# Kernel optimization log

Hardware: AMD Instinct MI355X
Metric: run time of the kernel (lower is better)

The kernel has to match this reference:

```python
import jax, jax.numpy as jnp
import numpy as np

B, V, M, L, D, OUT = 16, 16, 32, 24, 128, 193
VOCAB = {'cond': 5000, 'proc': 2000, 'drug': 600, 'lab_item': 700, 'lab_value': 200, 'inj_item': 400, 'inj_value': 200}


def setup_inputs() -> dict:
    key = jax.random.key(0)
    ks = iter(jax.random.split(key, 48))
    def emb_table(v):
        t = 0.02 * jax.random.normal(next(ks), (v, D), jnp.float32)
        return t.at[0].set(0.0)  # padding_idx = 0
    inp = {}
    inp['tok_cond'] = jax.random.randint(next(ks), (B, V, L), 0, VOCAB['cond'])
    inp['tok_proc'] = jax.random.randint(next(ks), (B, V, L), 0, VOCAB['proc'])
    inp['tok_drug'] = jax.random.randint(next(ks), (B, V, L), 0, VOCAB['drug'])
    inp['tok_lab_item'] = jax.random.randint(next(ks), (B, V, M, L), 0, VOCAB['lab_item'])
    inp['tok_lab_value'] = jax.random.randint(next(ks), (B, V, M, L), 0, VOCAB['lab_value'])
    inp['tok_inj_item'] = jax.random.randint(next(ks), (B, V, M, L), 0, VOCAB['inj_item'])
    inp['tok_inj_value'] = jax.random.randint(next(ks), (B, V, M, L), 0, VOCAB['inj_value'])
    inp['weight'] = jax.random.uniform(next(ks), (B, V, 1), jnp.float32)
    inp['age'] = jax.random.uniform(next(ks), (B, V, 1), jnp.float32)
    for n in ['cond', 'proc', 'drug', 'lab_item', 'lab_value', 'inj_item', 'inj_value']:
        inp['emb_' + n] = emb_table(VOCAB[n])
    def gru_params(nk):
        s = 0.05
        return (s * jax.random.normal(next(ks), (nk, 3 * D, D), jnp.float32),
                s * jax.random.normal(next(ks), (nk, 3 * D, D), jnp.float32),
                jnp.zeros((nk, 3 * D), jnp.float32),
                jnp.zeros((nk, 3 * D), jnp.float32))
    inp['mgru_wih'], inp['mgru_whh'], inp['mgru_bih'], inp['mgru_bhh'] = gru_params(5)
    inp['vgru_wih'], inp['vgru_whh'], inp['vgru_bih'], inp['vgru_bhh'] = gru_params(7)
    inp['info_w'] = 0.05 * jax.random.normal(next(ks), (2, D), jnp.float32)  # Linear(1, D) weights for weight/age
    inp['info_b'] = jnp.zeros((2, D), jnp.float32)
    inp['fc_w'] = 0.05 * jax.random.normal(next(ks), (7 * D, OUT), jnp.float32)
    inp['fc_b'] = jnp.zeros((OUT,), jnp.float32)
    return inp


def _gru(x, wih, whh, bih, bhh):
    # x: [N, T, Din]; torch nn.GRU semantics, gate order (r, z, n), h0 = 0
    n_, t_, _ = x.shape
    d = whh.shape[1]
    xg = jnp.einsum('ntd,gd->ntg', x, wih) + bih  # precompute input gates [N, T, 3D]
    def step(h, xg_t):
        gh = h @ whh.T + bhh
        ir, iz, inn = jnp.split(xg_t, 3, axis=-1)
        hr, hz, hn = jnp.split(gh, 3, axis=-1)
        r = jax.nn.sigmoid(ir + hr)
        z = jax.nn.sigmoid(iz + hz)
        n = jnp.tanh(inn + r * hn)
        h2 = (1.0 - z) * n + z * h
        return h2, h2
    h0 = jnp.zeros((n_, d), x.dtype)
    hT, outs = jax.lax.scan(step, h0, jnp.swapaxes(xg, 0, 1))
    return jnp.swapaxes(outs, 0, 1), hT  # output [N,T,D], hidden [N,D]

_gru_keys = jax.vmap(_gru)  # vmap over the per-feature-key leading axis


def reference(tok_cond, tok_proc, tok_drug, tok_lab_item, tok_lab_value, tok_inj_item, tok_inj_value,
              weight, age, emb_cond, emb_proc, emb_drug, emb_lab_item, emb_lab_value, emb_inj_item,
              emb_inj_value, mgru_wih, mgru_whh, mgru_bih, mgru_bhh, vgru_wih, vgru_whh, vgru_bih,
              vgru_bhh, info_w, info_b, fc_w, fc_b):
    b, v, m, _ = tok_lab_item.shape
    d = emb_cond.shape[1]
    # visit-event features: embedding + sum over code dim (dropout = identity, eval mode)
    e_cond = emb_cond[tok_cond].sum(axis=2)  # [B,V,D]
    e_proc = emb_proc[tok_proc].sum(axis=2)
    e_drug = emb_drug[tok_drug].sum(axis=2)
    # monitor-event pairs: elementwise mul of the two embeddings, sum over code dim
    lab = (emb_lab_item[tok_lab_item] * emb_lab_value[tok_lab_value]).sum(axis=3)  # [B,V,M,D]
    inj = (emb_inj_item[tok_inj_item] * emb_inj_value[tok_inj_value]).sum(axis=3)
    # repeat visit embeddings across the monitor axis (repeat(1, max_monitors, 1))
    rep = lambda e: jnp.broadcast_to(e[:, :, None, :], (b, v, m, d))
    mon_in = jnp.stack([rep(e_cond), rep(e_proc), rep(e_drug), lab, inj], axis=0)
    mon_in = mon_in.reshape(5, b * v, m, d)  # aggregate_tensors with uniform lengths
    # per-key monitor-level GRUs
    mon_out, mon_h = _gru_keys(mon_in, mgru_wih, mgru_whh, mgru_bih, mgru_bhh)
    # split_tensor + extract_and_transpose: take last monitor step per visit -> [5,B,V,D]
    last = mon_out[:, :, -1, :].reshape(5, b, v, d)
    # patient info Linear(1, D) for weight / age
    w_emb = weight * info_w[0] + info_b[0]  # [B,V,D]
    a_emb = age * info_w[1] + info_b[1]
    vis_in = jnp.concatenate([last, jnp.stack([w_emb, a_emb], axis=0)], axis=0)  # [7,B,V,D]
    # per-key visit-level GRUs
    _, vis_h = _gru_keys(vis_in, vgru_wih, vgru_whh, vgru_bih, vgru_bhh)  # [7,B,D]
    patient_emb = jnp.transpose(vis_h, (1, 0, 2)).reshape(b, 7 * d)  # concatenate_patient_embeddings
    logits = jax.nn.relu(patient_emb) @ fc_w + fc_b  # fc_patient: ReLU -> Linear(7D, output_size)
    return logits
```

## Files before the change

kernel.cpp:

```cpp
#include <hip/hip_runtime.h>
#include <stdint.h>

typedef unsigned short u16;
typedef unsigned int u32;

#define B_ 16
#define V_ 16
#define M_ 32
#define L_ 24
#define D_ 128
#define G_ 384
#define N_ 256
#define NM_ 8192
#define OUT_ 193

using bf16x8 = __attribute__((ext_vector_type(8))) __bf16;
using floatx4 = __attribute__((ext_vector_type(4))) float;
using u16x4 = __attribute__((ext_vector_type(4))) u16;

__device__ __forceinline__ float bf2f(u16 u) {
  u32 x = ((u32)u) << 16;
  return __builtin_bit_cast(float, x);
}
__device__ __forceinline__ u16 f2bf(float f) {
  u32 u = __builtin_bit_cast(u32, f);
  u = (u + 0x7FFFu + ((u >> 16) & 1u)) >> 16;
  return (u16)u;
}
__device__ __forceinline__ float sigm_(float x) {
  return __builtin_amdgcn_rcpf(1.0f + __expf(-x));
}
__device__ __forceinline__ float tanh_(float x) {
  float e = __expf(2.0f * x);
  return 1.0f - 2.0f * __builtin_amdgcn_rcpf(e + 1.0f);
}
__device__ __forceinline__ floatx4 mfma16(bf16x8 a, bf16x8 b, floatx4 c) {
  return __builtin_amdgcn_mfma_f32_16x16x32_bf16(a, b, c, 0, 0, 0);
}
__device__ __forceinline__ void lds_barrier() {
  asm volatile("s_waitcnt lgkmcnt(0)\n\ts_barrier" ::: "memory");
}

__device__ __forceinline__ void split4(floatx4 v, u16* __restrict__ hip, u16* __restrict__ lop) {
  u16x4 h, l;
#pragma unroll
  for (int k = 0; k < 4; k++) {
    u16 hb = f2bf(v[k]);
    h[k] = hb;
    l[k] = f2bf(v[k] - bf2f(hb));
  }
  *(u16x4*)hip = h;
  *(u16x4*)lop = l;
}

#define CONVB 1152
#define VEB 32
#define PEB 1024

__global__ __launch_bounds__(256) void k_stage1(
    const int* __restrict__ tc, const int* __restrict__ tp, const int* __restrict__ td,
    const int* __restrict__ tli, const int* __restrict__ tlv,
    const int* __restrict__ tii, const int* __restrict__ tiv,
    const float* __restrict__ ec, const float* __restrict__ ep, const float* __restrict__ ed,
    const float* __restrict__ eli, const float* __restrict__ elv,
    const float* __restrict__ eii, const float* __restrict__ eiv,
    const float* __restrict__ wv, const float* __restrict__ av,
    const float* __restrict__ iw, const float* __restrict__ ib,
    const float* __restrict__ mwih, const float* __restrict__ vwih,
    const float* __restrict__ mwhh, const float* __restrict__ vwhh,
    u16* __restrict__ wih_hi, u16* __restrict__ whh_hi,
    u16* __restrict__ ce_hi, u16* __restrict__ ce_lo,
    u16* __restrict__ vx_hi, u16* __restrict__ vx_lo,
    u16* __restrict__ mx_hi, u16* __restrict__ mx_lo) {
  int blk = blockIdx.x, tid = threadIdx.x;
  if (blk < CONVB) {
    const int SW = 12 * G_ * D_, S5 = 5 * G_ * D_;
    int i4 = (blk * 256 + tid) * 4;
    floatx4 v;
    u16* dst;
    if (i4 < SW) {
      v = *(const floatx4*)(i4 < S5 ? mwih + i4 : vwih + (i4 - S5));
      dst = wih_hi + i4;
    } else {
      int o = i4 - SW;
      v = *(const floatx4*)(o < S5 ? mwhh + o : vwhh + (o - S5));
      dst = whh_hi + o;
    }
    u16x4 h;
#pragma unroll
    for (int k = 0; k < 4; k++) h[k] = f2bf(v[k]);
    *(u16x4*)dst = h;
  } else if (blk < CONVB + VEB) {
    int n = (blk - CONVB) * 8 + (tid >> 5);
    int j = tid & 31;
    floatx4 a0 = {0.f, 0.f, 0.f, 0.f}, a1 = a0, a2 = a0;
#pragma unroll 4
    for (int l = 0; l < L_; l++) {
      a0 += *(const floatx4*)(ec + (size_t)tc[n * L_ + l] * D_ + j * 4);
      a1 += *(const floatx4*)(ep + (size_t)tp[n * L_ + l] * D_ + j * 4);
      a2 += *(const floatx4*)(ed + (size_t)td[n * L_ + l] * D_ + j * 4);
    }
    size_t o0 = (size_t)n * D_ + j * 4;
    split4(a0, ce_hi + o0, ce_lo + o0);
    split4(a1, ce_hi + (size_t)N_ * D_ + o0, ce_lo + (size_t)N_ * D_ + o0);
    split4(a2, ce_hi + (size_t)2 * N_ * D_ + o0, ce_lo + (size_t)2 * N_ * D_ + o0);
    float wq = wv[n], aq = av[n];
    floatx4 iw0 = *(const floatx4*)(iw + j * 4);
    floatx4 iw1 = *(const floatx4*)(iw + D_ + j * 4);
    floatx4 ib0 = *(const floatx4*)(ib + j * 4);
    floatx4 ib1 = *(const floatx4*)(ib + D_ + j * 4);
    floatx4 v1 = wq * iw0 + ib0;
    floatx4 v2 = aq * iw1 + ib1;
    split4(v1, vx_hi + (size_t)5 * N_ * D_ + o0, vx_lo + (size_t)5 * N_ * D_ + o0);
    split4(v2, vx_hi + (size_t)6 * N_ * D_ + o0, vx_lo + (size_t)6 * N_ * D_ + o0);
  } else {
    int r = (blk - CONVB - VEB) * 8 + (tid >> 5);
    int j = tid & 31;
    floatx4 al4 = {0.f, 0.f, 0.f, 0.f}, ai4 = al4;
#pragma unroll 4
    for (int l = 0; l < L_; l++) {
      al4 += *(const floatx4*)(eli + (size_t)tli[r * L_ + l] * D_ + j * 4) *
             *(const floatx4*)(elv + (size_t)tlv[r * L_ + l] * D_ + j * 4);
      ai4 += *(const floatx4*)(eii + (size_t)tii[r * L_ + l] * D_ + j * 4) *
             *(const floatx4*)(eiv + (size_t)tiv[r * L_ + l] * D_ + j * 4);
    }
    size_t o = (size_t)r * D_ + j * 4;
    split4(al4, mx_hi + o, mx_lo + o);
    split4(ai4, mx_hi + (size_t)NM_ * D_ + o, mx_lo + (size_t)NM_ * D_ + o);
  }
}

__global__ __launch_bounds__(256) void k_gemm_all(
    const u16* __restrict__ mx_hi, const u16* __restrict__ mx_lo,
    const u16* __restrict__ ce_hi, const u16* __restrict__ ce_lo,
    const u16* __restrict__ wih_hi, const float* __restrict__ mbih,
    float* __restrict__ xg_mon, float* __restrict__ xg_c) {
  int bid = blockIdx.x;
  int w = threadIdx.x >> 6, lane = threadIdx.x & 63;
  int mq = lane & 15, q = lane >> 4;
  const u16 *Ahb, *Alb, *Wk;
  const float* bias;
  float* out;
  int row, cb;
  if (bid < 1024) {
    int key = bid >> 9, rem = bid & 511;
    row = (rem >> 2) * 64 + w * 16;
    cb = (rem & 3) * 96;
    Ahb = mx_hi + (size_t)key * NM_ * D_;
    Alb = mx_lo + (size_t)key * NM_ * D_;
    Wk = wih_hi + (size_t)(3 + key) * G_ * D_;
    bias = mbih + (3 + key) * G_;
    out = xg_mon + (size_t)key * NM_ * G_;
  } else {
    int b2 = bid - 1024;
    int key = b2 >> 4, rem = b2 & 15;
    row = (rem >> 2) * 64 + w * 16;
    cb = (rem & 3) * 96;
    Ahb = ce_hi + (size_t)key * N_ * D_;
    Alb = ce_lo + (size_t)key * N_ * D_;
    Wk = wih_hi + (size_t)key * G_ * D_;
    bias = mbih + key * G_;
    out = xg_c + (size_t)key * N_ * G_;
  }

  bf16x8 wf[6][4];
#pragma unroll
  for (int j = 0; j < 6; j++)
#pragma unroll
    for (int kk = 0; kk < 4; kk++)
      wf[j][kk] = *(const bf16x8*)(Wk + (size_t)(cb + j * 16 + mq) * D_ + kk * 32 + q * 8);

  const u16* Ah = Ahb + (size_t)(row + mq) * D_;
  const u16* Al = Alb + (size_t)(row + mq) * D_;
  bf16x8 ah[4], al[4];
#pragma unroll
  for (int kk = 0; kk < 4; kk++) {
    ah[kk] = *(const bf16x8*)(Ah + kk * 32 + q * 8);
    al[kk] = *(const bf16x8*)(Al + kk * 32 + q * 8);
  }

  floatx4 acc[6];
#pragma unroll
  for (int j = 0; j < 6; j++) {
    float bv = bias[cb + j * 16 + mq];
    acc[j] = {bv, bv, bv, bv};
  }
#pragma unroll
  for (int j = 0; j < 6; j++)
#pragma unroll
    for (int kk = 0; kk < 4; kk++) {
      acc[j] = mfma16(ah[kk], wf[j][kk], acc[j]);
      acc[j] = mfma16(al[kk], wf[j][kk], acc[j]);
    }

  float* op = out + (size_t)(row + q * 4) * G_ + cb + mq;
#pragma unroll
  for (int j = 0; j < 6; j++)
#pragma unroll
    for (int i = 0; i < 4; i++) op[(size_t)i * G_ + j * 16] = acc[j][i];
}

__global__ __launch_bounds__(256) void k_gemm_xg(
    const u16* __restrict__ A_hi, const u16* __restrict__ A_lo,
    const u16* __restrict__ W_hi,
    const float* __restrict__ bias,
    float* __restrict__ out, int A_ks, int W_ks, int b_ks, int o_ks) {
  int key = blockIdx.z;
  int w = threadIdx.x >> 6, lane = threadIdx.x & 63;
  int mq = lane & 15, q = lane >> 4;
  int row = blockIdx.x * 64 + w * 16;
  int cb = blockIdx.y * 96;

  const u16* Wk = W_hi + (size_t)key * W_ks;
  bf16x8 wf[6][4];
#pragma unroll
  for (int j = 0; j < 6; j++)
#pragma unroll
    for (int kk = 0; kk < 4; kk++)
      wf[j][kk] = *(const bf16x8*)(Wk + (size_t)(cb + j * 16 + mq) * D_ + kk * 32 + q * 8);

  const u16* Ah = A_hi + (size_t)key * A_ks + (size_t)(row + mq) * D_;
  const u16* Al = A_lo + (size_t)key * A_ks + (size_t)(row + mq) * D_;
  bf16x8 ah[4], al[4];
#pragma unroll
  for (int kk = 0; kk < 4; kk++) {
    ah[kk] = *(const bf16x8*)(Ah + kk * 32 + q * 8);
    al[kk] = *(const bf16x8*)(Al + kk * 32 + q * 8);
  }

  floatx4 acc[6];
#pragma unroll
  for (int j = 0; j < 6; j++) {
    float bv = bias[key * b_ks + cb + j * 16 + mq];
    acc[j] = {bv, bv, bv, bv};
  }
#pragma unroll
  for (int j = 0; j < 6; j++)
#pragma unroll
    for (int kk = 0; kk < 4; kk++) {
      acc[j] = mfma16(ah[kk], wf[j][kk], acc[j]);
      acc[j] = mfma16(al[kk], wf[j][kk], acc[j]);
    }

  float* op = out + (size_t)key * o_ks + (size_t)(row + q * 4) * G_ + cb + mq;
#pragma unroll
  for (int j = 0; j < 6; j++)
#pragma unroll
    for (int i = 0; i < 4; i++) op[(size_t)i * G_ + j * 16] = acc[j][i];
}

template <int MODE, int TT>
__global__ __launch_bounds__(512, 1) void k_gru8(
    int cpk, const float* __restrict__ xg_a, const float* __restrict__ xg_b,
    const u16* __restrict__ whh_all, const float* __restrict__ bhh_all,
    u16* __restrict__ out_hi, u16* __restrict__ out_lo, float* __restrict__ out_f32) {
  int key = blockIdx.x / cpk;
  int chunk = blockIdx.x % cpk;
  int n0 = chunk * 16;
  const u16* whh = whh_all + (size_t)key * (G_ * D_);
  const float* bhh = bhh_all + (size_t)key * G_;

  __shared__ u16 hls[2][2][16 * 128];

  int tid = threadIdx.x;
  int w = tid >> 6, lane = tid & 63, mq = lane & 15, q = lane >> 4;
  int dA = (w << 4) + mq;

  bf16x8 bw[3][4];
#pragma unroll
  for (int g = 0; g < 3; g++)
#pragma unroll
    for (int kk = 0; kk < 4; kk++)
      bw[g][kk] = *(const bf16x8*)(whh + (size_t)(g * 128 + dA) * D_ + kk * 32 + q * 8);

  floatx4 bseed[3];
#pragma unroll
  for (int g = 0; g < 3; g++) {
    float b = bhh[g * 128 + dA];
    bseed[g] = {b, b, b, b};
  }

  const float* xbase;
  size_t RS, TS;
  if (MODE == 0) {
    if (key < 3) { xbase = xg_a + ((size_t)key * N_ + n0) * G_; RS = G_; TS = 0; }
    else { xbase = xg_b + ((size_t)(key - 3) * NM_ + (size_t)n0 * M_) * G_; RS = (size_t)M_ * G_; TS = G_; }
  } else {
    xbase = xg_a + (size_t)key * N_ * G_; RS = (size_t)16 * G_; TS = G_;
  }
  const float* rowp[4];
#pragma unroll
  for (int i = 0; i < 4; i++) rowp[i] = xbase + (size_t)(q * 4 + i) * RS + dA;

  float xs[4][12];
#pragma unroll
  for (int s = 0; s < 3; s++) {
    int ts = s < TT ? s : TT - 1;
#pragma unroll
    for (int i = 0; i < 4; i++)
#pragma unroll
      for (int g = 0; g < 3; g++)
        xs[s][i * 3 + g] = rowp[i][(size_t)ts * TS + g * 128];
  }

  float h_old[4];
#pragma unroll
  for (int k = 0; k < 4; k++) h_old[k] = 0.f;

#define GRU_STEP(P)                                                                        \
  {                                                                                        \
    int t = tb + (P);                                                                      \
    {                                                                                      \
      int tpf = t + 3 < TT ? t + 3 : TT - 1;                                               \
      size_t to = (size_t)tpf * TS;                                                        \
      _Pragma("unroll") for (int i = 0; i < 4; i++)                                        \
          _Pragma("unroll") for (int g = 0; g < 3; g++)                                    \
              xs[((P) + 3) & 3][i * 3 + g] = rowp[i][to + g * 128];                        \
    }                                                                                      \
    floatx4 acc[3];                                                                        \
    if (t > 0) {                                                                           \
      const u16* hp0 = &hls[(t - 1) & 1][0][0];                                            \
      const u16* hp1 = &hls[(t - 1) & 1][1][0];                                            \
      bf16x8 ah[4], al[4];                                                                 \
      _Pragma("unroll") for (int kk = 0; kk < 4; kk++) {                                   \
        int off = mq * 128 + (((kk * 4 + q) ^ mq) * 8);                                    \
        ah[kk] = *(const bf16x8*)(hp0 + off);                                              \
        al[kk] = *(const bf16x8*)(hp1 + off);                                              \
      }                                                                                    \
      _Pragma("unroll") for (int g = 0; g < 3; g++) {                                      \
        floatx4 a = mfma16(ah[0], bw[g][0], bseed[g]);                                     \
        a = mfma16(al[0], bw[g][0], a);                                                    \
        a = mfma16(ah[1], bw[g][1], a);                                                    \
        a = mfma16(al[1], bw[g][1], a);                                                    \
        a = mfma16(ah[2], bw[g][2], a);                                                    \
        a = mfma16(al[2], bw[g][2], a);                                                    \
        a = mfma16(ah[3], bw[g][3], a);                                                    \
        acc[g] = mfma16(al[3], bw[g][3], a);                                               \
      }                                                                                    \
    } else {                                                                               \
      _Pragma("unroll") for (int g = 0; g < 3; g++) acc[g] = bseed[g];                     \
    }                                                                                      \
    u16* wrh = &hls[t & 1][0][0];                                                          \
    u16* wrl = &hls[t & 1][1][0];                                                          \
    _Pragma("unroll") for (int i = 0; i < 4; i++) {                                        \
      int row = q * 4 + i;                                                                 \
      float r = sigm_(xs[P][i * 3 + 0] + acc[0][i]);                                       \
      float z = sigm_(xs[P][i * 3 + 1] + acc[1][i]);                                       \
      float nn = tanh_(xs[P][i * 3 + 2] + r * acc[2][i]);                                  \
      float h2 = (1.0f - z) * nn + z * h_old[i];                                           \
      h_old[i] = h2;                                                                       \
      u32 ub = __builtin_bit_cast(u32, h2);                                                \
      u16 hb = (u16)(ub >> 16);                                                            \
      float rem = h2 - __builtin_bit_cast(float, ub & 0xFFFF0000u);                        \
      u16 lb = f2bf(rem);                                                                  \
      if (t == TT - 1) {                                                                   \
        if (MODE == 0) {                                                                   \
          size_t o = ((size_t)key * N_ + n0 + row) * D_ + dA;                              \
          out_hi[o] = hb;                                                                  \
          out_lo[o] = lb;                                                                  \
        } else {                                                                           \
          out_f32[((size_t)key * 16 + row) * D_ + dA] = h2;                                \
        }                                                                                  \
      } else {                                                                             \
        int idx = row * 128 + (((dA >> 3) ^ row) * 8) + (dA & 7);                          \
        wrh[idx] = hb;                                                                     \
        wrl[idx] = lb;                                                                     \
      }                                                                                    \
    }                                                                                      \
    if (t + 1 < TT) lds_barrier();                                                         \
  }

#pragma unroll 1
  for (int tb = 0; tb < TT; tb += 4) {
    GRU_STEP(0)
    GRU_STEP(1)
    GRU_STEP(2)
    GRU_STEP(3)
  }
#undef GRU_STEP
}

__global__ __launch_bounds__(256) void k_fc(
    const float* __restrict__ vis_h, const float* __restrict__ fc_w,
    const float* __restrict__ fc_b, float* __restrict__ out) {
  int b = blockIdx.x;
  int cg = blockIdx.y;
  int tid = threadIdx.x;
  int j = tid & 15, s = tid >> 4;
  int c = cg * 16 + j;
  bool cv = c < OUT_;

  __shared__ float hbuf[7 * D_];
  __shared__ float red[16][16];
  for (int i = tid; i < 7 * D_; i += 256) {
    float v = vis_h[((size_t)(i >> 7) * 16 + b) * D_ + (i & 127)];
    hbuf[i] = v > 0.f ? v : 0.f;
  }
  __syncthreads();

  float acc = 0.f;
  if (cv) {
    const float* wp = fc_w + (size_t)(s * 56) * OUT_ + c;
#pragma unroll 8
    for (int k = 0; k < 56; k++) acc += hbuf[s * 56 + k] * wp[(size_t)k * OUT_];
  }
  red[s][j] = acc;
  __syncthreads();
  if (s == 0 && cv) {
    float t = 0.f;
#pragma unroll
    for (int m = 0; m < 16; m++) t += red[m][j];
    out[(size_t)b * OUT_ + c] = t + fc_b[c];
  }
}

extern "C" void kernel_launch(void* const* d_in, const int* in_sizes, int n_in,
                              void* d_out, int out_size, void* d_ws, size_t ws_size,
                              hipStream_t stream) {
  (void)in_sizes; (void)n_in; (void)out_size; (void)ws_size;
  const int* tok_cond = (const int*)d_in[0];
  const int* tok_proc = (const int*)d_in[1];
  const int* tok_drug = (const int*)d_in[2];
  const int* tok_lab_item = (const int*)d_in[3];
  const int* tok_lab_value = (const int*)d_in[4];
  const int* tok_inj_item = (const int*)d_in[5];
  const int* tok_inj_value = (const int*)d_in[6];
  const float* weight = (const float*)d_in[7];
  const float* age = (const float*)d_in[8];
  const float* emb_cond = (const float*)d_in[9];
  const float* emb_proc = (const float*)d_in[10];
  const float* emb_drug = (const float*)d_in[11];
  const float* emb_lab_item = (const float*)d_in[12];
  const float* emb_lab_value = (const float*)d_in[13];
  const float* emb_inj_item = (const float*)d_in[14];
  const float* emb_inj_value = (const float*)d_in[15];
  const float* mgru_wih = (const float*)d_in[16];
  const float* mgru_whh = (const float*)d_in[17];
  const float* mgru_bih = (const float*)d_in[18];
  const float* mgru_bhh = (const float*)d_in[19];
  const float* vgru_wih = (const float*)d_in[20];
  const float* vgru_whh = (const float*)d_in[21];
  const float* vgru_bih = (const float*)d_in[22];
  const float* vgru_bhh = (const float*)d_in[23];
  const float* info_w = (const float*)d_in[24];
  const float* info_b = (const float*)d_in[25];
  const float* fc_w = (const float*)d_in[26];
  const float* fc_b = (const float*)d_in[27];

  char* p = (char*)d_ws;
  auto take = [&](size_t bytes) { char* r = p; p += (bytes + 255) & ~(size_t)255; return r; };
  u16* mx_hi = (u16*)take((size_t)2 * NM_ * D_ * 2);
  u16* mx_lo = (u16*)take((size_t)2 * NM_ * D_ * 2);
  u16* ce_hi = (u16*)take((size_t)3 * N_ * D_ * 2);
  u16* ce_lo = (u16*)take((size_t)3 * N_ * D_ * 2);
  u16* vx_hi = (u16*)take((size_t)7 * N_ * D_ * 2);
  u16* vx_lo = (u16*)take((size_t)7 * N_ * D_ * 2);
  float* xg_mon = (float*)take((size_t)2 * NM_ * G_ * 4);
  float* xg_c = (float*)take((size_t)3 * N_ * G_ * 4);
  float* xg_v = (float*)take((size_t)7 * N_ * G_ * 4);
  float* vis_h = (float*)take((size_t)7 * 16 * D_ * 4);
  u16* wih_hi = (u16*)take((size_t)12 * G_ * D_ * 2);
  u16* whh_hi = (u16*)take((size_t)12 * G_ * D_ * 2);

  k_stage1<<<CONVB + VEB + PEB, 256, 0, stream>>>(
      tok_cond, tok_proc, tok_drug, tok_lab_item, tok_lab_value, tok_inj_item, tok_inj_value,
      emb_cond, emb_proc, emb_drug, emb_lab_item, emb_lab_value, emb_inj_item, emb_inj_value,
      weight, age, info_w, info_b, mgru_wih, vgru_wih, mgru_whh, vgru_whh,
      wih_hi, whh_hi, ce_hi, ce_lo, vx_hi, vx_lo, mx_hi, mx_lo);
  k_gemm_all<<<1024 + 48, 256, 0, stream>>>(
      mx_hi, mx_lo, ce_hi, ce_lo, wih_hi, mgru_bih, xg_mon, xg_c);
  k_gru8<0, 32><<<80, 512, 0, stream>>>(16, xg_c, xg_mon, whh_hi, mgru_bhh,
                                        vx_hi, vx_lo, nullptr);
  k_gemm_xg<<<dim3(N_ / 64, 4, 7), 256, 0, stream>>>(
      vx_hi, vx_lo, wih_hi + (size_t)5 * G_ * D_,
      vgru_bih, xg_v, N_ * D_, G_ * D_, G_, N_ * G_);
  k_gru8<1, 16><<<7, 512, 0, stream>>>(1, xg_v, nullptr, whh_hi + (size_t)5 * G_ * D_, vgru_bhh,
                                       nullptr, nullptr, vis_h);
  k_fc<<<dim3(B_, 13), 256, 0, stream>>>(vis_h, fc_w, fc_b, (float*)d_out);
}
```

Baseline: 218.7 us.

## Fuse input-gate GEMM into GRU recurrence kernels with async LDS staging

Removes the separate input-projection GEMM kernels and their fp32 gate buffers, and computes x·Wih inside the recurrent GRU kernel with MFMA each timestep. Per-step inputs are loaded via global_load_lds into a double-buffered shared tile. Constant inputs (the repeated visit keys) are projected only once. This saves two launches and large global traffic, but adds MFMA work to the serial per-step critical path of an 80-block kernel. It also swaps the custom waitcnt barrier for __syncthreads.

```diff
diff --git a/kernel.cpp b/kernel.cpp
--- a/kernel.cpp
+++ b/kernel.cpp
@@ -37,8 +37,10 @@
 __device__ __forceinline__ floatx4 mfma16(bf16x8 a, bf16x8 b, floatx4 c) {
   return __builtin_amdgcn_mfma_f32_16x16x32_bf16(a, b, c, 0, 0, 0);
 }
-__device__ __forceinline__ void lds_barrier() {
-  asm volatile("s_waitcnt lgkmcnt(0)\n\ts_barrier" ::: "memory");
+__device__ __forceinline__ void stage16(const u16* gsrc, u16* ldst) {
+  __builtin_amdgcn_global_load_lds(
+      (const __attribute__((address_space(1))) void*)gsrc,
+      (__attribute__((address_space(3))) void*)ldst, 16, 0, 0);
 }
 
 __device__ __forceinline__ void split4(floatx4 v, u16* __restrict__ hip, u16* __restrict__ lop) {
@@ -130,254 +132,177 @@
   }
 }
 
-__global__ __launch_bounds__(256) void k_gemm_all(
-    const u16* __restrict__ mx_hi, const u16* __restrict__ mx_lo,
-    const u16* __restrict__ ce_hi, const u16* __restrict__ ce_lo,
-    const u16* __restrict__ wih_hi, const float* __restrict__ mbih,
-    float* __restrict__ xg_mon, float* __restrict__ xg_c) {
-  int bid = blockIdx.x;
-  int w = threadIdx.x >> 6, lane = threadIdx.x & 63;
-  int mq = lane & 15, q = lane >> 4;
-  const u16 *Ahb, *Alb, *Wk;
-  const float* bias;
-  float* out;
-  int row, cb;
-  if (bid < 1024) {
-    int key = bid >> 9, rem = bid & 511;
-    row = (rem >> 2) * 64 + w * 16;
-    cb = (rem & 3) * 96;
-    Ahb = mx_hi + (size_t)key * NM_ * D_;
-    Alb = mx_lo + (size_t)key * NM_ * D_;
-    Wk = wih_hi + (size_t)(3 + key) * G_ * D_;
-    bias = mbih + (3 + key) * G_;
-    out = xg_mon + (size_t)key * NM_ * G_;
-  } else {
-    int b2 = bid - 1024;
-    int key = b2 >> 4, rem = b2 & 15;
-    row = (rem >> 2) * 64 + w * 16;
-    cb = (rem & 3) * 96;
-    Ahb = ce_hi + (size_t)key * N_ * D_;
-    Alb = ce_lo + (size_t)key * N_ * D_;
-    Wk = wih_hi + (size_t)key * G_ * D_;
-    bias = mbih + key * G_;
-    out = xg_c + (size_t)key * N_ * G_;
-  }
-
-  bf16x8 wf[6][4];
-#pragma unroll
-  for (int j = 0; j < 6; j++)
-#pragma unroll
-    for (int kk = 0; kk < 4; kk++)
-      wf[j][kk] = *(const bf16x8*)(Wk + (size_t)(cb + j * 16 + mq) * D_ + kk * 32 + q * 8);
-
-  const u16* Ah = Ahb + (size_t)(row + mq) * D_;
-  const u16* Al = Alb + (size_t)(row + mq) * D_;
-  bf16x8 ah[4], al[4];
-#pragma unroll
-  for (int kk = 0; kk < 4; kk++) {
-    ah[kk] = *(const bf16x8*)(Ah + kk * 32 + q * 8);
-    al[kk] = *(const bf16x8*)(Al + kk * 32 + q * 8);
-  }
-
-  floatx4 acc[6];
-#pragma unroll
-  for (int j = 0; j < 6; j++) {
-    float bv = bias[cb + j * 16 + mq];
-    acc[j] = {bv, bv, bv, bv};
-  }
-#pragma unroll
-  for (int j = 0; j < 6; j++)
-#pragma unroll
-    for (int kk = 0; kk < 4; kk++) {
-      acc[j] = mfma16(ah[kk], wf[j][kk], acc[j]);
-      acc[j] = mfma16(al[kk], wf[j][kk], acc[j]);
-    }
-
-  float* op = out + (size_t)(row + q * 4) * G_ + cb + mq;
-#pragma unroll
-  for (int j = 0; j < 6; j++)
-#pragma unroll
-    for (int i = 0; i < 4; i++) op[(size_t)i * G_ + j * 16] = acc[j][i];
-}
-
-__global__ __launch_bounds__(256) void k_gemm_xg(
-    const u16* __restrict__ A_hi, const u16* __restrict__ A_lo,
-    const u16* __restrict__ W_hi,
-    const float* __restrict__ bias,
-    float* __restrict__ out, int A_ks, int W_ks, int b_ks, int o_ks) {
-  int key = blockIdx.z;
-  int w = threadIdx.x >> 6, lane = threadIdx.x & 63;
-  int mq = lane & 15, q = lane >> 4;
-  int row = blockIdx.x * 64 + w * 16;
-  int cb = blockIdx.y * 96;
-
-  const u16* Wk = W_hi + (size_t)key * W_ks;
-  bf16x8 wf[6][4];
-#pragma unroll
-  for (int j = 0; j < 6; j++)
-#pragma unroll
-    for (int kk = 0; kk < 4; kk++)
-      wf[j][kk] = *(const bf16x8*)(Wk + (size_t)(cb + j * 16 + mq) * D_ + kk * 32 + q * 8);
-
-  const u16* Ah = A_hi + (size_t)key * A_ks + (size_t)(row + mq) * D_;
-  const u16* Al = A_lo + (size_t)key * A_ks + (size_t)(row + mq) * D_;
-  bf16x8 ah[4], al[4];
-#pragma unroll
-  for (int kk = 0; kk < 4; kk++) {
-    ah[kk] = *(const bf16x8*)(Ah + kk * 32 + q * 8);
-    al[kk] = *(const bf16x8*)(Al + kk * 32 + q * 8);
-  }
-
-  floatx4 acc[6];
-#pragma unroll
-  for (int j = 0; j < 6; j++) {
-    float bv = bias[key * b_ks + cb + j * 16 + mq];
-    acc[j] = {bv, bv, bv, bv};
-  }
-#pragma unroll
-  for (int j = 0; j < 6; j++)
-#pragma unroll
-    for (int kk = 0; kk < 4; kk++) {
-      acc[j] = mfma16(ah[kk], wf[j][kk], acc[j]);
-      acc[j] = mfma16(al[kk], wf[j][kk], acc[j]);
-    }
-
-  float* op = out + (size_t)key * o_ks + (size_t)(row + q * 4) * G_ + cb + mq;
-#pragma unroll
-  for (int j = 0; j < 6; j++)
-#pragma unroll
-    for (int i = 0; i < 4; i++) op[(size_t)i * G_ + j * 16] = acc[j][i];
-}
-
 template <int MODE, int TT>
 __global__ __launch_bounds__(512, 1) void k_gru8(
-    int cpk, const float* __restrict__ xg_a, const float* __restrict__ xg_b,
+    int cpk,
+    const u16* __restrict__ xa_hi, const u16* __restrict__ xa_lo,
+    const u16* __restrict__ xb_hi, const u16* __restrict__ xb_lo,
+    const u16* __restrict__ wih_all, const float* __restrict__ bih_all,
     const u16* __restrict__ whh_all, const float* __restrict__ bhh_all,
     u16* __restrict__ out_hi, u16* __restrict__ out_lo, float* __restrict__ out_f32) {
   int key = blockIdx.x / cpk;
-  int chunk = blockIdx.x % cpk;
+  int chunk = blockIdx.x - key * cpk;
   int n0 = chunk * 16;
   const u16* whh = whh_all + (size_t)key * (G_ * D_);
-  const float* bhh = bhh_all + (size_t)key * G_;
-
-  __shared__ u16 hls[2][2][16 * 128];
+  const u16* wih = wih_all + (size_t)key * (G_ * D_);
+
+  __shared__ __align__(16) u16 hls[2][2][16 * 128];
+  __shared__ __align__(16) u16 xls[2][2][16 * 128];
 
   int tid = threadIdx.x;
   int w = tid >> 6, lane = tid & 63, mq = lane & 15, q = lane >> 4;
   int dA = (w << 4) + mq;
 
-  bf16x8 bw[3][4];
+  int sp = tid >> 8, sr = (tid >> 4) & 15, sc = tid & 15;
+  u16* ldst0 = &xls[0][0][0] + (size_t)sp * (16 * 128) + (sr * 16 + sc) * 8;
+  u16* ldst1 = &xls[1][0][0] + (size_t)sp * (16 * 128) + (sr * 16 + sc) * 8;
+  const bool constx = (MODE == 0) && (key < 3);
+  const u16* gsrc;
+  {
+    const u16* hi;
+    const u16* lo;
+    size_t grow;
+    if (MODE == 0) {
+      if (key < 3) { hi = xa_hi; lo = xa_lo; grow = (size_t)key * N_ + n0 + sr; }
+      else         { hi = xb_hi; lo = xb_lo; grow = (size_t)(key - 3) * NM_ + (size_t)(n0 + sr) * M_; }
+    } else {
+      hi = xa_hi; lo = xa_lo; grow = (size_t)key * N_ + sr * 16;
+    }
+    gsrc = (sp ? lo : hi) + grow * D_ + ((sc ^ sr) * 8);
+  }
+
+  bf16x8 bw[3][4], wf[3][4];
 #pragma unroll
   for (int g = 0; g < 3; g++)
 #pragma unroll
-    for (int kk = 0; kk < 4; kk++)
-      bw[g][kk] = *(const bf16x8*)(whh + (size_t)(g * 128 + dA) * D_ + kk * 32 + q * 8);
-
-  floatx4 bseed[3];
+    for (int kk = 0; kk < 4; kk++) {
+      size_t ro = (size_t)(g * 128 + dA) * D_ + kk * 32 + q * 8;
+      bw[g][kk] = *(const bf16x8*)(whh + ro);
+      wf[g][kk] = *(const bf16x8*)(wih + ro);
+    }
+  floatx4 bseed[3], bxs[3];
 #pragma unroll
   for (int g = 0; g < 3; g++) {
-    float b = bhh[g * 128 + dA];
-    bseed[g] = {b, b, b, b};
-  }
-
-  const float* xbase;
-  size_t RS, TS;
-  if (MODE == 0) {
-    if (key < 3) { xbase = xg_a + ((size_t)key * N_ + n0) * G_; RS = G_; TS = 0; }
-    else { xbase = xg_b + ((size_t)(key - 3) * NM_ + (size_t)n0 * M_) * G_; RS = (size_t)M_ * G_; TS = G_; }
-  } else {
-    xbase = xg_a + (size_t)key * N_ * G_; RS = (size_t)16 * G_; TS = G_;
-  }
-  const float* rowp[4];
-#pragma unroll
-  for (int i = 0; i < 4; i++) rowp[i] = xbase + (size_t)(q * 4 + i) * RS + dA;
-
-  float xs[4][12];
-#pragma unroll
-  for (int s = 0; s < 3; s++) {
-    int ts = s < TT ? s : TT - 1;
-#pragma unroll
-    for (int i = 0; i < 4; i++)
-#pragma unroll
-      for (int g = 0; g < 3; g++)
-        xs[s][i * 3 + g] = rowp[i][(size_t)ts * TS + g * 128];
+    float bh = bhh_all[key * G_ + g * 128 + dA];
+    float bi = bih_all[key * G_ + g * 128 + dA];
+    bseed[g] = {bh, bh, bh, bh};
+    bxs[g] = {bi, bi, bi, bi};
+  }
+
+  stage16(gsrc, ldst0);
+  __syncthreads();
+
+  floatx4 accx[3];
+  if (constx) {
+    const u16* xp0 = &xls[0][0][0];
+    const u16* xp1 = &xls[0][1][0];
+    bf16x8 xh[4], xl[4];
+#pragma unroll
+    for (int kk = 0; kk < 4; kk++) {
+      int off = mq * 128 + (((kk * 4 + q) ^ mq) * 8);
+      xh[kk] = *(const bf16x8*)(xp0 + off);
+      xl[kk] = *(const bf16x8*)(xp1 + off);
+    }
+#pragma unroll
+    for (int g = 0; g < 3; g++) {
+      floatx4 a = mfma16(xh[0], wf[g][0], bxs[g]);
+      a = mfma16(xl[0], wf[g][0], a);
+      a = mfma16(xh[1], wf[g][1], a);
+      a = mfma16(xl[1], wf[g][1], a);
+      a = mfma16(xh[2], wf[g][2], a);
+      a = mfma16(xl[2], wf[g][2], a);
+      a = mfma16(xh[3], wf[g][3], a);
+      accx[g] = mfma16(xl[3], wf[g][3], a);
+    }
   }
 
   float h_old[4];
 #pragma unroll
   for (int k = 0; k < 4; k++) h_old[k] = 0.f;
 
-#define GRU_STEP(P)                                                                        \
-  {                                                                                        \
-    int t = tb + (P);                                                                      \
-    {                                                                                      \
-      int tpf = t + 3 < TT ? t + 3 : TT - 1;                                               \
-      size_t to = (size_t)tpf * TS;                                                        \
-      _Pragma("unroll") for (int i = 0; i < 4; i++)                                        \
-          _Pragma("unroll") for (int g = 0; g < 3; g++)                                    \
-              xs[((P) + 3) & 3][i * 3 + g] = rowp[i][to + g * 128];                        \
-    }                                                                                      \
-    floatx4 acc[3];                                                                        \
-    if (t > 0) {                                                                           \
-      const u16* hp0 = &hls[(t - 1) & 1][0][0];                                            \
-      const u16* hp1 = &hls[(t - 1) & 1][1][0];                                            \
-      bf16x8 ah[4], al[4];                                                                 \
-      _Pragma("unroll") for (int kk = 0; kk < 4; kk++) {                                   \
-        int off = mq * 128 + (((kk * 4 + q) ^ mq) * 8);                                    \
-        ah[kk] = *(const bf16x8*)(hp0 + off);                                              \
-        al[kk] = *(const bf16x8*)(hp1 + off);                                              \
-      }                                                                                    \
-      _Pragma("unroll") for (int g = 0; g < 3; g++) {                                      \
-        floatx4 a = mfma16(ah[0], bw[g][0], bseed[g]);                                     \
-        a = mfma16(al[0], bw[g][0], a);                                                    \
-        a = mfma16(ah[1], bw[g][1], a);                                                    \
-        a = mfma16(al[1], bw[g][1], a);                                                    \
-        a = mfma16(ah[2], bw[g][2], a);                                                    \
-        a = mfma16(al[2], bw[g][2], a);                                                    \
-        a = mfma16(ah[3], bw[g][3], a);                                                    \
-        acc[g] = mfma16(al[3], bw[g][3], a);                                               \
-      }                                                                                    \
-    } else {                                                                               \
-      _Pragma("unroll") for (int g = 0; g < 3; g++) acc[g] = bseed[g];                     \
-    }                                                                                      \
-    u16* wrh = &hls[t & 1][0][0];                                                          \
-    u16* wrl = &hls[t & 1][1][0];                                                          \
-    _Pragma("unroll") for (int i = 0; i < 4; i++) {                                        \
-      int row = q * 4 + i;                                                                 \
-      float r = sigm_(xs[P][i * 3 + 0] + acc[0][i]);                                       \
-      float z = sigm_(xs[P][i * 3 + 1] + acc[1][i]);                                       \
-      float nn = tanh_(xs[P][i * 3 + 2] + r * acc[2][i]);                                  \
-      float h2 = (1.0f - z) * nn + z * h_old[i];                                           \
-      h_old[i] = h2;                                                                       \
-      u32 ub = __builtin_bit_cast(u32, h2);                                                \
-      u16 hb = (u16)(ub >> 16);                                                            \
-      float rem = h2 - __builtin_bit_cast(float, ub & 0xFFFF0000u);                        \
-      u16 lb = f2bf(rem);                                                                  \
-      if (t == TT - 1) {                                                                   \
-        if (MODE == 0) {                                                                   \
-          size_t o = ((size_t)key * N_ + n0 + row) * D_ + dA;                              \
-          out_hi[o] = hb;                                                                  \
-          out_lo[o] = lb;                                                                  \
-        } else {                                                                           \
-          out_f32[((size_t)key * 16 + row) * D_ + dA] = h2;                                \
-        }                                                                                  \
-      } else {                                                                             \
-        int idx = row * 128 + (((dA >> 3) ^ row) * 8) + (dA & 7);                          \
-        wrh[idx] = hb;                                                                     \
-        wrl[idx] = lb;                                                                     \
-      }                                                                                    \
-    }                                                                                      \
-    if (t + 1 < TT) lds_barrier();                                                         \
-  }
-
-#pragma unroll 1
-  for (int tb = 0; tb < TT; tb += 4) {
-    GRU_STEP(0)
-    GRU_STEP(1)
-    GRU_STEP(2)
-    GRU_STEP(3)
-  }
-#undef GRU_STEP
+#pragma unroll 2
+  for (int t = 0; t < TT; ++t) {
+    int slot = t & 1;
+    if (!constx && (t + 1 < TT))
+      stage16(gsrc + (size_t)(t + 1) * D_, slot ? ldst0 : ldst1);
+    if (!constx) {
+      const u16* xp0 = &xls[slot][0][0];
+      const u16* xp1 = &xls[slot][1][0];
+      bf16x8 xh[4], xl[4];
+#pragma unroll
+      for (int kk = 0; kk < 4; kk++) {
+        int off = mq * 128 + (((kk * 4 + q) ^ mq) * 8);
+        xh[kk] = *(const bf16x8*)(xp0 + off);
+        xl[kk] = *(const bf16x8*)(xp1 + off);
+      }
+#pragma unroll
+      for (int g = 0; g < 3; g++) {
+        floatx4 a = mfma16(xh[0], wf[g][0], bxs[g]);
+        a = mfma16(xl[0], wf[g][0], a);
+        a = mfma16(xh[1], wf[g][1], a);
+        a = mfma16(xl[1], wf[g][1], a);
+        a = mfma16(xh[2], wf[g][2], a);
+        a = mfma16(xl[2], wf[g][2], a);
+        a = mfma16(xh[3], wf[g][3], a);
+        accx[g] = mfma16(xl[3], wf[g][3], a);
+      }
+    }
+    floatx4 acch[3];
+    if (t > 0) {
+      const u16* hp0 = &hls[(t - 1) & 1][0][0];
+      const u16* hp1 = &hls[(t - 1) & 1][1][0];
+      bf16x8 ah[4], al[4];
+#pragma unroll
+      for (int kk = 0; kk < 4; kk++) {
+        int off = mq * 128 + (((kk * 4 + q) ^ mq) * 8);
+        ah[kk] = *(const bf16x8*)(hp0 + off);
+        al[kk] = *(const bf16x8*)(hp1 + off);
+      }
+#pragma unroll
+      for (int g = 0; g < 3; g++) {
+        floatx4 a = mfma16(ah[0], bw[g][0], bseed[g]);
+        a = mfma16(al[0], bw[g][0], a);
+        a = mfma16(ah[1], bw[g][1], a);
+        a = mfma16(al[1], bw[g][1], a);
+        a = mfma16(ah[2], bw[g][2], a);
+        a = mfma16(al[2], bw[g][2], a);
+        a = mfma16(ah[3], bw[g][3], a);
+        acch[g] = mfma16(al[3], bw[g][3], a);
+      }
+    } else {
+#pragma unroll
+      for (int g = 0; g < 3; g++) acch[g] = bseed[g];
+    }
+    u16* wrh = &hls[slot][0][0];
+    u16* wrl = &hls[slot][1][0];
+#pragma unroll
+    for (int i = 0; i < 4; i++) {
+      int row = q * 4 + i;
+      float r = sigm_(accx[0][i] + acch[0][i]);
+      float z = sigm_(accx[1][i] + acch[1][i]);
+      float nn = tanh_(accx[2][i] + r * acch[2][i]);
+      float h2 = (1.0f - z) * nn + z * h_old[i];
+      h_old[i] = h2;
+      u32 ub = __builtin_bit_cast(u32, h2);
+      u16 hb = (u16)(ub >> 16);
+      float rem = h2 - __builtin_bit_cast(float, ub & 0xFFFF0000u);
+      u16 lb = f2bf(rem);
+      if (t == TT - 1) {
+        if (MODE == 0) {
+          size_t o = ((size_t)key * N_ + n0 + row) * D_ + dA;
+          out_hi[o] = hb;
+          out_lo[o] = lb;
+        } else {
+          out_f32[((size_t)key * 16 + row) * D_ + dA] = h2;
+        }
+      } else {
+        int idx = row * 128 + (((dA >> 3) ^ row) * 8) + (dA & 7);
+        wrh[idx] = hb;
+        wrl[idx] = lb;
+      }
+    }
+    if (t + 1 < TT) __syncthreads();
+  }
 }
 
 __global__ __launch_bounds__(256) void k_fc(
@@ -455,9 +380,6 @@
   u16* ce_lo = (u16*)take((size_t)3 * N_ * D_ * 2);
   u16* vx_hi = (u16*)take((size_t)7 * N_ * D_ * 2);
   u16* vx_lo = (u16*)take((size_t)7 * N_ * D_ * 2);
-  float* xg_mon = (float*)take((size_t)2 * NM_ * G_ * 4);
-  float* xg_c = (float*)take((size_t)3 * N_ * G_ * 4);
-  float* xg_v = (float*)take((size_t)7 * N_ * G_ * 4);
   float* vis_h = (float*)take((size_t)7 * 16 * D_ * 4);
   u16* wih_hi = (u16*)take((size_t)12 * G_ * D_ * 2);
   u16* whh_hi = (u16*)take((size_t)12 * G_ * D_ * 2);
@@ -467,14 +389,12 @@
       emb_cond, emb_proc, emb_drug, emb_lab_item, emb_lab_value, emb_inj_item, emb_inj_value,
       weight, age, info_w, info_b, mgru_wih, vgru_wih, mgru_whh, vgru_whh,
       wih_hi, whh_hi, ce_hi, ce_lo, vx_hi, vx_lo, mx_hi, mx_lo);
-  k_gemm_all<<<1024 + 48, 256, 0, stream>>>(
-      mx_hi, mx_lo, ce_hi, ce_lo, wih_hi, mgru_bih, xg_mon, xg_c);
-  k_gru8<0, 32><<<80, 512, 0, stream>>>(16, xg_c, xg_mon, whh_hi, mgru_bhh,
+  k_gru8<0, 32><<<80, 512, 0, stream>>>(16, ce_hi, ce_lo, mx_hi, mx_lo,
+                                        wih_hi, mgru_bih, whh_hi, mgru_bhh,
                                         vx_hi, vx_lo, nullptr);
-  k_gemm_xg<<<dim3(N_ / 64, 4, 7), 256, 0, stream>>>(
-      vx_hi, vx_lo, wih_hi + (size_t)5 * G_ * D_,
-      vgru_bih, xg_v, N_ * D_, G_ * D_, G_, N_ * G_);
-  k_gru8<1, 16><<<7, 512, 0, stream>>>(1, xg_v, nullptr, whh_hi + (size_t)5 * G_ * D_, vgru_bhh,
+  k_gru8<1, 16><<<7, 512, 0, stream>>>(1, vx_hi, vx_lo, nullptr, nullptr,
+                                       wih_hi + (size_t)5 * G_ * D_, vgru_bih,
+                                       whh_hi + (size_t)5 * G_ * D_, vgru_bhh,
                                        nullptr, nullptr, vis_h);
   k_fc<<<dim3(B_, 13), 256, 0, stream>>>(vis_h, fc_w, fc_b, (float*)d_out);
 }
```

New measurement: 224.5 us. +2.7%, slower.
